# Performance work log

Measured on AMD Instinct MI355X. Metric: run time of the kernel, lower is better.

The kernel has to match this reference:

```python
import jax, jax.numpy as jnp
import numpy as np

TAU = 2.0
V_THRESHOLD = 1.0
V_RESET = 0.0
TIME_STEPS = 16
SG_ALPHA = 4.0  # spikingjelly surrogate.Sigmoid default alpha


@jax.custom_vjp
def spike_fn(x):
    # heaviside forward, sigmoid surrogate backward (spikingjelly default)
    return (x >= 0.0).astype(x.dtype)

def _spike_fwd(x):
    return spike_fn(x), x

def _spike_bwd(x, g):
    s = jax.nn.sigmoid(SG_ALPHA * x)
    return (g * SG_ALPHA * s * (1.0 - s),)

spike_fn.defvjp(_spike_fwd, _spike_bwd)


def setup_inputs() -> dict:
    key = jax.random.key(0)
    k1, k2, k3 = jax.random.split(key, 3)
    B, D_in, D_h = 32768, 512, 512
    bound = 1.0 / np.sqrt(D_in)
    x = jax.random.normal(k1, (B, D_in), dtype=jnp.float32)
    W = jax.random.uniform(k2, (D_h, D_in), dtype=jnp.float32, minval=-bound, maxval=bound)
    b = jax.random.uniform(k3, (D_h,), dtype=jnp.float32, minval=-bound, maxval=bound)
    return {"x": x, "W": W, "b": b}


def reference(x, W, b):
    # fc(x) is identical every timestep in the original loop; compute once.
    cur = jnp.dot(x, W.T) + b  # [B, H]

    v0 = jnp.full_like(cur, V_RESET)
    acc0 = jnp.zeros_like(cur)

    def step(carry, _):
        v, acc = carry
        # LIF charge (decay_input=True): v = v + (x - (v - v_reset)) / tau
        v = v + (cur - (v - V_RESET)) / TAU
        spk = spike_fn(v - V_THRESHOLD)
        # hard reset, detach_reset=True
        spk_d = jax.lax.stop_gradient(spk)
        v = (1.0 - spk_d) * v + spk_d * V_RESET
        return (v, acc + spk), None

    (v, acc), _ = jax.lax.scan(step, (v0, acc0), None, length=TIME_STEPS)
    return acc / TIME_STEPS
```

## Files before the change

### kernel.cpp

```cpp
#include <hip/hip_runtime.h>


typedef float v4f __attribute__((ext_vector_type(4)));

#define BM 256
#define BN 128
#define BK 16
#define LDA (BM + 4)
#define LDB (BN + 4)

__global__ __launch_bounds__(256, 2)
void lif_gemm_f32(const float* __restrict__ x,
                  const float* __restrict__ W,
                  const float* __restrict__ bias,
                  float* __restrict__ out,
                  int K, int H)
{
    __shared__ __align__(16) float As[2][BK][LDA];
    __shared__ __align__(16) float Bs[2][BK][LDB];

    const int tid = threadIdx.x;
    const int tm  = tid & 15;
    const int tn  = tid >> 4;
    const int n0  = blockIdx.x * BN;
    const int m0  = blockIdx.y * BM;

    const int ra = tid >> 1;
    const int kc = (tid & 1) << 3;

    const float* xg  = x + (size_t)(m0 + ra) * K + kc;
    const float* xg2 = xg + (size_t)128 * K;
    const float* wg  = W + (size_t)(n0 + ra) * K + kc;

    float acc[16][8];
#pragma unroll
    for (int i = 0; i < 16; ++i)
#pragma unroll
        for (int j = 0; j < 8; ++j)
            acc[i][j] = 0.0f;

    v4f a0 = *(const v4f*)(xg);
    v4f a1 = *(const v4f*)(xg + 4);
    v4f a2 = *(const v4f*)(xg2);
    v4f a3 = *(const v4f*)(xg2 + 4);
    v4f b0 = *(const v4f*)(wg);
    v4f b1 = *(const v4f*)(wg + 4);

    int pp = 0;
    for (int k0 = 0; k0 < K; k0 += BK) {
        float (*Asp)[LDA] = As[pp];
        float (*Bsp)[LDB] = Bs[pp];

#pragma unroll
        for (int i = 0; i < 4; ++i) {
            Asp[kc + i][ra]           = a0[i];
            Asp[kc + 4 + i][ra]       = a1[i];
            Asp[kc + i][128 + ra]     = a2[i];
            Asp[kc + 4 + i][128 + ra] = a3[i];
            Bsp[kc + i][ra]           = b0[i];
            Bsp[kc + 4 + i][ra]       = b1[i];
        }
        __syncthreads();

        const int kn = (k0 + BK < K) ? (k0 + BK) : k0;
        a0 = *(const v4f*)(xg + kn);
        a1 = *(const v4f*)(xg + kn + 4);
        a2 = *(const v4f*)(xg2 + kn);
        a3 = *(const v4f*)(xg2 + kn + 4);
        b0 = *(const v4f*)(wg + kn);
        b1 = *(const v4f*)(wg + kn + 4);

        v4f fa0[2], fa1[2], fa2[2], fa3[2], fb0[2], fb1[2];
        fa0[0] = *(const v4f*)&Asp[0][tm * 4];
        fa1[0] = *(const v4f*)&Asp[0][64 + tm * 4];
        fa2[0] = *(const v4f*)&Asp[0][128 + tm * 4];
        fa3[0] = *(const v4f*)&Asp[0][192 + tm * 4];
        fb0[0] = *(const v4f*)&Bsp[0][tn * 4];
        fb1[0] = *(const v4f*)&Bsp[0][64 + tn * 4];

#pragma unroll
        for (int k = 0; k < BK; ++k) {
            const int cb = k & 1, nb = cb ^ 1;
            if (k + 1 < BK) {
                fa0[nb] = *(const v4f*)&Asp[k + 1][tm * 4];
                fa1[nb] = *(const v4f*)&Asp[k + 1][64 + tm * 4];
                fa2[nb] = *(const v4f*)&Asp[k + 1][128 + tm * 4];
                fa3[nb] = *(const v4f*)&Asp[k + 1][192 + tm * 4];
                fb0[nb] = *(const v4f*)&Bsp[k + 1][tn * 4];
                fb1[nb] = *(const v4f*)&Bsp[k + 1][64 + tn * 4];
            }
#pragma unroll
            for (int i = 0; i < 16; ++i) {
                const float a = (i < 4) ? fa0[cb][i]
                              : (i < 8) ? fa1[cb][i - 4]
                              : (i < 12) ? fa2[cb][i - 8]
                              : fa3[cb][i - 12];
#pragma unroll
                for (int j = 0; j < 8; ++j) {
                    const float b = (j < 4) ? fb0[cb][j] : fb1[cb][j - 4];
                    acc[i][j] = fmaf(a, b, acc[i][j]);
                }
            }
        }
        pp ^= 1;
    }

    float bcol[8];
#pragma unroll
    for (int j = 0; j < 8; ++j) {
        const int col = (j < 4) ? (tn * 4 + j) : (64 + tn * 4 + (j - 4));
        bcol[j] = bias[n0 + col];
    }

#pragma unroll
    for (int i = 0; i < 16; ++i) {
        const int row = m0 + 64 * (i >> 2) + tm * 4 + (i & 3);
        float res[8];
#pragma unroll
        for (int j = 0; j < 8; ++j) {
            const float cur = acc[i][j] + bcol[j];
            float v = 0.0f;
            int cnt = 0;
#pragma unroll
            for (int t = 0; t < 16; ++t) {
                v = v + (cur - v) * 0.5f;
                const bool s = (v >= 1.0f);
                cnt += s ? 1 : 0;
                v = s ? 0.0f : v;
            }
            res[j] = (float)cnt * 0.0625f;
        }
        float* op = out + (size_t)row * H + n0;
        *(v4f*)(op + tn * 4)      = (v4f){res[0], res[1], res[2], res[3]};
        *(v4f*)(op + 64 + tn * 4) = (v4f){res[4], res[5], res[6], res[7]};
    }
}

extern "C" void kernel_launch(void* const* d_in, const int* in_sizes, int n_in,
                              void* d_out, int out_size, void* d_ws, size_t ws_size,
                              hipStream_t stream) {
    const float* x    = (const float*)d_in[0];
    const float* W    = (const float*)d_in[1];
    const float* bias = (const float*)d_in[2];
    float* out = (float*)d_out;

    const int K = 512;
    const int H = 512;
    const int B = in_sizes[0] / K;

    dim3 grid(H / BN, B / BM);
    dim3 block(256);
    lif_gemm_f32<<<grid, block, 0, stream>>>(x, W, bias, out, K, H);
}
```

Baseline: 306.7 us.

## Stage only x tiles in LDS and read W wave-uniformly from global memory

Reworks the GEMM tiling to 512x64 block tiles. Each wave owns 16 output columns and reads its W values directly from global memory through a wave-uniform pointer, prefetched two k at a time and meant to become scalar loads, so B no longer goes through LDS. Each lane computes 8 rows by 16 columns and stores four contiguous v4f per row. The goal is to remove the LDS traffic and bank-transpose stores for B and raise the reuse of A per LDS read, at the cost of relying on scalar or cached global loads for W. The grid order also changes so that blocks sharing W columns run near each other.

```diff
diff --git a/kernel.cpp b/kernel.cpp
--- a/kernel.cpp
+++ b/kernel.cpp
@@ -2,123 +2,123 @@
 
 
 typedef float v4f __attribute__((ext_vector_type(4)));
+typedef float v2f __attribute__((ext_vector_type(2)));
 
-#define BM 256
-#define BN 128
+#define KK 512
+#define HH 512
+#define BM 512
+#define BN 64
 #define BK 16
-#define LDA (BM + 4)
-#define LDB (BN + 4)
 
 __global__ __launch_bounds__(256, 2)
 void lif_gemm_f32(const float* __restrict__ x,
                   const float* __restrict__ W,
                   const float* __restrict__ bias,
-                  float* __restrict__ out,
-                  int K, int H)
+                  float* __restrict__ out)
 {
-    __shared__ __align__(16) float As[2][BK][LDA];
-    __shared__ __align__(16) float Bs[2][BK][LDB];
+    __shared__ __align__(16) float As[2][BK][BM];
 
-    const int tid = threadIdx.x;
-    const int tm  = tid & 15;
-    const int tn  = tid >> 4;
-    const int n0  = blockIdx.x * BN;
-    const int m0  = blockIdx.y * BM;
+    const int tid  = threadIdx.x;
+    const int lane = tid & 63;
+    const int wv   = __builtin_amdgcn_readfirstlane(tid >> 6);
+    const int m0   = blockIdx.x * BM;
+    const int n0   = blockIdx.y * BN + wv * 16;
 
     const int ra = tid >> 1;
     const int kc = (tid & 1) << 3;
+    const float* xg = x + (size_t)(m0 + ra) * KK + kc;
 
-    const float* xg  = x + (size_t)(m0 + ra) * K + kc;
-    const float* xg2 = xg + (size_t)128 * K;
-    const float* wg  = W + (size_t)(n0 + ra) * K + kc;
+    const float* wrow = W + (size_t)n0 * KK;
 
-    float acc[16][8];
+    float acc[8][16];
 #pragma unroll
-    for (int i = 0; i < 16; ++i)
+    for (int i = 0; i < 8; ++i)
 #pragma unroll
-        for (int j = 0; j < 8; ++j)
-            acc[i][j] = 0.0f;
+        for (int c = 0; c < 16; ++c) acc[i][c] = 0.0f;
 
-    v4f a0 = *(const v4f*)(xg);
-    v4f a1 = *(const v4f*)(xg + 4);
-    v4f a2 = *(const v4f*)(xg2);
-    v4f a3 = *(const v4f*)(xg2 + 4);
-    v4f b0 = *(const v4f*)(wg);
-    v4f b1 = *(const v4f*)(wg + 4);
+    v4f g[4][2];
+#pragma unroll
+    for (int p = 0; p < 4; ++p) {
+        g[p][0] = *(const v4f*)(xg + p * 128 * KK);
+        g[p][1] = *(const v4f*)(xg + p * 128 * KK + 4);
+    }
+
+    v2f bb0[16], bb1[16];
+#pragma unroll
+    for (int c = 0; c < 16; ++c)
+        bb0[c] = *(const v2f*)(wrow + c * KK);
 
     int pp = 0;
-    for (int k0 = 0; k0 < K; k0 += BK) {
-        float (*Asp)[LDA] = As[pp];
-        float (*Bsp)[LDB] = Bs[pp];
+    for (int k0 = 0; k0 < KK; k0 += BK) {
+        float (*Asp)[BM] = As[pp];
 
 #pragma unroll
-        for (int i = 0; i < 4; ++i) {
-            Asp[kc + i][ra]           = a0[i];
-            Asp[kc + 4 + i][ra]       = a1[i];
-            Asp[kc + i][128 + ra]     = a2[i];
-            Asp[kc + 4 + i][128 + ra] = a3[i];
-            Bsp[kc + i][ra]           = b0[i];
-            Bsp[kc + 4 + i][ra]       = b1[i];
-        }
+        for (int p = 0; p < 4; ++p)
+#pragma unroll
+            for (int i = 0; i < 8; ++i)
+                Asp[kc + i][ra + 128 * p] = (i < 4) ? g[p][0][i] : g[p][1][i - 4];
         __syncthreads();
 
-        const int kn = (k0 + BK < K) ? (k0 + BK) : k0;
-        a0 = *(const v4f*)(xg + kn);
-        a1 = *(const v4f*)(xg + kn + 4);
-        a2 = *(const v4f*)(xg2 + kn);
-        a3 = *(const v4f*)(xg2 + kn + 4);
-        b0 = *(const v4f*)(wg + kn);
-        b1 = *(const v4f*)(wg + kn + 4);
+        const int kn = (k0 + BK < KK) ? (k0 + BK) : k0;
+#pragma unroll
+        for (int p = 0; p < 4; ++p) {
+            g[p][0] = *(const v4f*)(xg + p * 128 * KK + kn);
+            g[p][1] = *(const v4f*)(xg + p * 128 * KK + kn + 4);
+        }
 
-        v4f fa0[2], fa1[2], fa2[2], fa3[2], fb0[2], fb1[2];
-        fa0[0] = *(const v4f*)&Asp[0][tm * 4];
-        fa1[0] = *(const v4f*)&Asp[0][64 + tm * 4];
-        fa2[0] = *(const v4f*)&Asp[0][128 + tm * 4];
-        fa3[0] = *(const v4f*)&Asp[0][192 + tm * 4];
-        fb0[0] = *(const v4f*)&Bsp[0][tn * 4];
-        fb1[0] = *(const v4f*)&Bsp[0][64 + tn * 4];
+        v4f fa[2][2];
+        fa[0][0] = *(const v4f*)&Asp[0][lane * 8];
+        fa[0][1] = *(const v4f*)&Asp[0][lane * 8 + 4];
 
 #pragma unroll
-        for (int k = 0; k < BK; ++k) {
-            const int cb = k & 1, nb = cb ^ 1;
-            if (k + 1 < BK) {
-                fa0[nb] = *(const v4f*)&Asp[k + 1][tm * 4];
-                fa1[nb] = *(const v4f*)&Asp[k + 1][64 + tm * 4];
-                fa2[nb] = *(const v4f*)&Asp[k + 1][128 + tm * 4];
-                fa3[nb] = *(const v4f*)&Asp[k + 1][192 + tm * 4];
-                fb0[nb] = *(const v4f*)&Bsp[k + 1][tn * 4];
-                fb1[nb] = *(const v4f*)&Bsp[k + 1][64 + tn * 4];
+        for (int kp = 0; kp < 8; ++kp) {
+            const int knb0 = k0 + 2 * kp + 2;
+            const int knb  = (knb0 <= KK - 2) ? knb0 : (KK - 2);
+            if (kp & 1) {
+#pragma unroll
+                for (int c = 0; c < 16; ++c)
+                    bb0[c] = *(const v2f*)(wrow + c * KK + knb);
+            } else {
+#pragma unroll
+                for (int c = 0; c < 16; ++c)
+                    bb1[c] = *(const v2f*)(wrow + c * KK + knb);
             }
+
 #pragma unroll
-            for (int i = 0; i < 16; ++i) {
-                const float a = (i < 4) ? fa0[cb][i]
-                              : (i < 8) ? fa1[cb][i - 4]
-                              : (i < 12) ? fa2[cb][i - 8]
-                              : fa3[cb][i - 12];
+            for (int h = 0; h < 2; ++h) {
+                const int k  = 2 * kp + h;
+                const int cb = k & 1;
+                const int nb = cb ^ 1;
+                if (k + 1 < BK) {
+                    fa[nb][0] = *(const v4f*)&Asp[k + 1][lane * 8];
+                    fa[nb][1] = *(const v4f*)&Asp[k + 1][lane * 8 + 4];
+                }
 #pragma unroll
-                for (int j = 0; j < 8; ++j) {
-                    const float b = (j < 4) ? fb0[cb][j] : fb1[cb][j - 4];
-                    acc[i][j] = fmaf(a, b, acc[i][j]);
+                for (int i = 0; i < 8; ++i) {
+                    const float a = (i < 4) ? fa[cb][0][i] : fa[cb][1][i - 4];
+#pragma unroll
+                    for (int c = 0; c < 16; ++c) {
+                        const float b = (kp & 1) ? bb1[c][h] : bb0[c][h];
+                        acc[i][c] = fmaf(a, b, acc[i][c]);
+                    }
                 }
             }
         }
         pp ^= 1;
     }
 
-    float bcol[8];
+    float bs[16];
 #pragma unroll
-    for (int j = 0; j < 8; ++j) {
-        const int col = (j < 4) ? (tn * 4 + j) : (64 + tn * 4 + (j - 4));
-        bcol[j] = bias[n0 + col];
-    }
+    for (int c = 0; c < 16; ++c)
+        bs[c] = bias[n0 + c];
 
+    const int rbase = m0 + lane * 8;
 #pragma unroll
-    for (int i = 0; i < 16; ++i) {
-        const int row = m0 + 64 * (i >> 2) + tm * 4 + (i & 3);
-        float res[8];
+    for (int i = 0; i < 8; ++i) {
+        float res[16];
 #pragma unroll
-        for (int j = 0; j < 8; ++j) {
-            const float cur = acc[i][j] + bcol[j];
+        for (int c = 0; c < 16; ++c) {
+            const float cur = acc[i][c] + bs[c];
             float v = 0.0f;
             int cnt = 0;
 #pragma unroll
@@ -128,11 +128,12 @@
                 cnt += s ? 1 : 0;
                 v = s ? 0.0f : v;
             }
-            res[j] = (float)cnt * 0.0625f;
+            res[c] = (float)cnt * 0.0625f;
         }
-        float* op = out + (size_t)row * H + n0;
-        *(v4f*)(op + tn * 4)      = (v4f){res[0], res[1], res[2], res[3]};
-        *(v4f*)(op + 64 + tn * 4) = (v4f){res[4], res[5], res[6], res[7]};
+        float* op = out + (size_t)(rbase + i) * HH + n0;
+#pragma unroll
+        for (int q = 0; q < 4; ++q)
+            *(v4f*)(op + q * 4) = (v4f){res[4*q], res[4*q+1], res[4*q+2], res[4*q+3]};
     }
 }
 
@@ -144,11 +145,9 @@
     const float* bias = (const float*)d_in[2];
     float* out = (float*)d_out;
 
-    const int K = 512;
-    const int H = 512;
-    const int B = in_sizes[0] / K;
+    const int B = in_sizes[0] / KK;
 
-    dim3 grid(H / BN, B / BM);
+    dim3 grid(B / BM, HH / BN);
     dim3 block(256);
-    lif_gemm_f32<<<grid, block, 0, stream>>>(x, W, bias, out, K, H);
+    lif_gemm_f32<<<grid, block, 0, stream>>>(x, W, bias, out);
 }
```

Result: slower. 445.4 us (+45.2%).
